# Performance work log

Measured on AMD Instinct MI355X. Metric: run time of the kernel, lower is better.

The kernel has to match this reference:

```python
import jax, jax.numpy as jnp
import numpy as np

N = 100000   # nodes
E = 1600000  # edges (avg degree 16)
IN_DIM = 5
HID = 128
OUT_DIM = 1


def gcn_conv(x, src, dst, W, b, n):
    """PyG GCNConv: out = D^{-1/2}(A+I)D^{-1/2} (x @ W) + b, self-loops added."""
    h = x @ W  # [N, F_out]
    # degree including self-loop (edge weight 1 each)
    deg = jax.ops.segment_sum(jnp.ones(src.shape[0], h.dtype), dst, num_segments=n) + 1.0
    dinv = jax.lax.rsqrt(deg)  # deg >= 1 always (self-loop)
    coef = dinv[src] * dinv[dst]  # [E]
    agg = jax.ops.segment_sum(h[src] * coef[:, None], dst, num_segments=n)
    agg = agg + h * (dinv * dinv)[:, None]  # self-loop contribution
    return agg + b


def setup_inputs() -> dict:
    key = jax.random.key(0)
    k = jax.random.split(key, 6)
    x = jax.random.normal(k[0], (N, IN_DIM), jnp.float32)
    edge_index = jax.random.randint(k[1], (2, E), 0, N)
    W1 = jax.random.normal(k[2], (IN_DIM, HID), jnp.float32) / np.float32(np.sqrt(IN_DIM))
    b1 = jnp.zeros((HID,), jnp.float32)
    W2 = jax.random.normal(k[3], (HID, OUT_DIM), jnp.float32) / np.float32(np.sqrt(HID))
    b2 = jnp.zeros((OUT_DIM,), jnp.float32)
    return {"x": x, "edge_index": edge_index, "W1": W1, "b1": b1, "W2": W2, "b2": b2}


def reference(x, edge_index, W1, b1, W2, b2):
    src, dst = edge_index[0], edge_index[1]
    h = gcn_conv(x, src, dst, W1, b1, N)
    h = jax.nn.relu(h)
    out = gcn_conv(h, src, dst, W2, b2, N)
    return out
```

## Files before the change

### kernel.cpp

```cpp
#include <hip/hip_runtime.h>
#include <hip/hip_fp16.h>

#define Nn 100000
#define Ee 1600000
#define HID 128
#define IN_DIM 5

#define SH 8
#define BSZ 256
#define NB 391
#define BCAP 4608

#define PCHUNK 4000
#define PBLK (Ee / PCHUNK)

typedef float f32x4 __attribute__((ext_vector_type(4)));
union F2H { float f; __half2 h; };

__global__ void zero_kernel(int* __restrict__ bcnt) {
    if (threadIdx.x < NB) bcnt[threadIdx.x] = 0;
}

__global__ __launch_bounds__(512) void partition_kernel(const int* __restrict__ src,
                                                        const int* __restrict__ dst,
                                                        unsigned int* __restrict__ recs,
                                                        int* __restrict__ bcnt) {
    __shared__ unsigned int stage[PCHUNK];
    __shared__ int hist[NB + 1];
    __shared__ int cur[NB];
    __shared__ int gbase[NB];
    int e0 = blockIdx.x * PCHUNK;
    for (int i = threadIdx.x; i <= NB; i += 512) hist[i] = 0;
    __syncthreads();
    for (int e = e0 + threadIdx.x; e < e0 + PCHUNK; e += 512)
        atomicAdd(&hist[(dst[e] >> SH) + 1], 1);
    __syncthreads();
    if (threadIdx.x == 0)
        for (int b = 1; b <= NB; ++b) hist[b] += hist[b - 1];
    __syncthreads();
    if (threadIdx.x < NB) {
        int c0 = hist[threadIdx.x], c1 = hist[threadIdx.x + 1];
        cur[threadIdx.x] = c0;
        gbase[threadIdx.x] = atomicAdd(&bcnt[threadIdx.x], c1 - c0);
    }
    __syncthreads();
    for (int e = e0 + threadIdx.x; e < e0 + PCHUNK; e += 512) {
        int d = dst[e], s = src[e];
        int b = d >> SH;
        int slot = atomicAdd(&cur[b], 1);
        stage[slot] = ((unsigned int)(d & (BSZ - 1)) << 17) | (unsigned int)s;
    }
    __syncthreads();
    int wave = threadIdx.x >> 6, lane = threadIdx.x & 63;
    for (int b = wave; b < NB; b += 8) {
        int c0 = hist[b], len = hist[b + 1] - c0;
        unsigned int* o = recs + (size_t)b * BCAP + gbase[b];
        for (int i = lane; i < len; i += 64) o[i] = stage[c0 + i];
    }
}

__global__ __launch_bounds__(BSZ) void sortk_kernel(const unsigned int* __restrict__ recs,
                                                    const int* __restrict__ bcnt,
                                                    const float* __restrict__ x,
                                                    int* __restrict__ degc,
                                                    unsigned int* __restrict__ nodeoff,
                                                    unsigned int* __restrict__ ssrc,
                                                    float* __restrict__ dinv,
                                                    f32x4* __restrict__ xd16) {
    __shared__ int cnt[BSZ];
    __shared__ int cur[BSZ];
    __shared__ int wsum[BSZ / 64];
    int b = blockIdx.x, tid = threadIdx.x;
    int n = bcnt[b];
    cnt[tid] = 0;
    __syncthreads();
    const unsigned int* R = recs + (size_t)b * BCAP;
    for (int i = tid; i < n; i += BSZ)
        atomicAdd(&cnt[R[i] >> 17], 1);
    __syncthreads();
    int v = cnt[tid];
    int lane = tid & 63, wid = tid >> 6;
    int sc = v;
    #pragma unroll
    for (int ofs = 1; ofs < 64; ofs <<= 1) {
        int t = __shfl_up(sc, ofs, 64);
        if (lane >= ofs) sc += t;
    }
    if (lane == 63) wsum[wid] = sc;
    __syncthreads();
    int wpre = 0;
    #pragma unroll
    for (int w = 0; w < BSZ / 64; ++w)
        if (w < wid) wpre += wsum[w];
    int excl = wpre + sc - v;
    cur[tid] = excl;
    int g = (b << SH) + tid;
    if (g < Nn) {
        degc[g] = v;
        nodeoff[g] = (unsigned int)(b * BCAP + excl);
        float di = rsqrtf((float)v + 1.0f);
        dinv[g] = di;
        f32x4 o;
        o.x = x[g * IN_DIM + 0] * di;
        o.y = x[g * IN_DIM + 1] * di;
        o.z = x[g * IN_DIM + 2] * di;
        F2H u;
        u.h = __floats2half2_rn(x[g * IN_DIM + 3] * di, x[g * IN_DIM + 4] * di);
        o.w = u.f;
        xd16[g] = o;
    }
    __syncthreads();
    unsigned int* O = ssrc + (size_t)b * BCAP;
    for (int i = tid; i < n; i += BSZ) {
        unsigned int r = R[i];
        int pos = atomicAdd(&cur[r >> 17], 1);
        O[pos] = r & 0x1FFFFu;
    }
}

__global__ __launch_bounds__(256) void gcn1_kernel(const unsigned int* __restrict__ ssrc,
                                                   const unsigned int* __restrict__ nodeoff,
                                                   const int* __restrict__ degc,
                                                   const f32x4* __restrict__ xd16,
                                                   const float* __restrict__ dinv,
                                                   const float* __restrict__ W1,
                                                   const float* __restrict__ b1,
                                                   const float* __restrict__ W2,
                                                   float* __restrict__ h2d) {
    __shared__ float w1s[IN_DIM * HID];
    __shared__ float w2s[HID], b1s[HID];
    int tid = threadIdx.x;
    for (int j = tid; j < IN_DIM * HID; j += 256) w1s[j] = W1[j];
    if (tid < HID) { w2s[tid] = W2[tid]; b1s[tid] = b1[tid]; }
    __syncthreads();
    int nd = blockIdx.x * 256 + tid;
    if (nd >= Nn) return;
    unsigned int off = nodeoff[nd];
    int len = degc[nd];
    float a0 = 0.f, a1 = 0.f, a2 = 0.f, a3 = 0.f, a4 = 0.f;
    int i = 0;
    for (; i + 4 <= len; i += 4) {
        unsigned int s0 = ssrc[off + i], s1 = ssrc[off + i + 1];
        unsigned int s2 = ssrc[off + i + 2], s3 = ssrc[off + i + 3];
        f32x4 v0 = xd16[s0], v1 = xd16[s1], v2 = xd16[s2], v3 = xd16[s3];
        F2H u0, u1, u2, u3;
        u0.f = v0.w; u1.f = v1.w; u2.f = v2.w; u3.f = v3.w;
        float2 e0 = __half22float2(u0.h), e1 = __half22float2(u1.h);
        float2 e2 = __half22float2(u2.h), e3 = __half22float2(u3.h);
        a0 += (v0.x + v1.x) + (v2.x + v3.x);
        a1 += (v0.y + v1.y) + (v2.y + v3.y);
        a2 += (v0.z + v1.z) + (v2.z + v3.z);
        a3 += (e0.x + e1.x) + (e2.x + e3.x);
        a4 += (e0.y + e1.y) + (e2.y + e3.y);
    }
    for (; i < len; ++i) {
        unsigned int s = ssrc[off + i];
        f32x4 v = xd16[s];
        F2H u; u.f = v.w; float2 e = __half22float2(u.h);
        a0 += v.x; a1 += v.y; a2 += v.z; a3 += e.x; a4 += e.y;
    }
    float di = dinv[nd];
    f32x4 sv = xd16[nd];
    F2H su; su.f = sv.w; float2 se = __half22float2(su.h);
    a0 = (a0 + sv.x) * di;
    a1 = (a1 + sv.y) * di;
    a2 = (a2 + sv.z) * di;
    a3 = (a3 + se.x) * di;
    a4 = (a4 + se.y) * di;
    float accp = 0.f;
    #pragma unroll
    for (int f = 0; f < HID; ++f) {
        float v = b1s[f] + a0 * w1s[f] + a1 * w1s[HID + f] + a2 * w1s[2 * HID + f]
                + a3 * w1s[3 * HID + f] + a4 * w1s[4 * HID + f];
        accp += fmaxf(v, 0.f) * w2s[f];
    }
    h2d[nd] = accp * di;
}

__global__ __launch_bounds__(256) void gcn2_kernel(const unsigned int* __restrict__ ssrc,
                                                   const unsigned int* __restrict__ nodeoff,
                                                   const int* __restrict__ degc,
                                                   const float* __restrict__ h2d,
                                                   const float* __restrict__ dinv,
                                                   const float* __restrict__ b2,
                                                   float* __restrict__ out) {
    int nd = blockIdx.x * 256 + threadIdx.x;
    if (nd >= Nn) return;
    unsigned int off = nodeoff[nd];
    int len = degc[nd];
    float s = 0.f;
    int i = 0;
    for (; i + 8 <= len; i += 8) {
        float t0 = h2d[ssrc[off + i]],     t1 = h2d[ssrc[off + i + 1]];
        float t2 = h2d[ssrc[off + i + 2]], t3 = h2d[ssrc[off + i + 3]];
        float t4 = h2d[ssrc[off + i + 4]], t5 = h2d[ssrc[off + i + 5]];
        float t6 = h2d[ssrc[off + i + 6]], t7 = h2d[ssrc[off + i + 7]];
        s += ((t0 + t1) + (t2 + t3)) + ((t4 + t5) + (t6 + t7));
    }
    for (; i < len; ++i) s += h2d[ssrc[off + i]];
    out[nd] = (s + h2d[nd]) * dinv[nd] + b2[0];
}

extern "C" void kernel_launch(void* const* d_in, const int* in_sizes, int n_in,
                              void* d_out, int out_size, void* d_ws, size_t ws_size,
                              hipStream_t stream) {
    const float* x  = (const float*)d_in[0];
    const int*   ei = (const int*)d_in[1];
    const float* W1 = (const float*)d_in[2];
    const float* b1 = (const float*)d_in[3];
    const float* W2 = (const float*)d_in[4];
    const float* b2 = (const float*)d_in[5];
    const int* src = ei;
    const int* dst = ei + Ee;
    float* out = (float*)d_out;

    float* dinv = (float*)d_ws;
    f32x4* xd16 = (f32x4*)(dinv + Nn);
    float* h2d  = (float*)(xd16 + Nn);
    int* degc   = (int*)(h2d + Nn);
    unsigned int* nodeoff = (unsigned int*)(degc + Nn);
    unsigned int* recs = nodeoff + Nn;
    unsigned int* ssrc = recs + (size_t)NB * BCAP;
    int* bcnt = (int*)(ssrc + (size_t)NB * BCAP);

    zero_kernel<<<1, 512, 0, stream>>>(bcnt);
    partition_kernel<<<PBLK, 512, 0, stream>>>(src, dst, recs, bcnt);
    sortk_kernel<<<NB, BSZ, 0, stream>>>(recs, bcnt, x, degc, nodeoff, ssrc, dinv, xd16);
    gcn1_kernel<<<(Nn + 255) / 256, 256, 0, stream>>>(ssrc, nodeoff, degc, xd16, dinv,
                                                      W1, b1, W2, h2d);
    gcn2_kernel<<<(Nn + 255) / 256, 256, 0, stream>>>(ssrc, nodeoff, degc, h2d, dinv, b2, out);
}
```

Measured before the change: 81.87 us.

## Restructure edge partition: register-cached edges, parallel scan, flat coalesced scatter

The partition kernel now loads each edge's src/dst once into registers (up to 7 per thread) instead of reading dst twice from global memory. The serial single-thread prefix sum over 391 buckets becomes a wave-shuffle scan. The per-wave bucket copy-out becomes a flat loop over staged records, using an extra shared bucket-id array. Chunk size changes to 3125 with 512 blocks for better occupancy and more blocks in flight, at the cost of more global atomics on bucket counters.

Result: faster. 70.21 us (-14.2%).

```diff
diff --git a/kernel.cpp b/kernel.cpp
--- a/kernel.cpp
+++ b/kernel.cpp
@@ -11,8 +11,9 @@
 #define NB 391
 #define BCAP 4608
 
-#define PCHUNK 4000
-#define PBLK (Ee / PCHUNK)
+#define PCHUNK 3125
+#define PBLK 512
+#define MAXK 7
 
 typedef float f32x4 __attribute__((ext_vector_type(4)));
 union F2H { float f; __half2 h; };
@@ -26,36 +27,63 @@
                                                         unsigned int* __restrict__ recs,
                                                         int* __restrict__ bcnt) {
     __shared__ unsigned int stage[PCHUNK];
+    __shared__ unsigned short bstage[PCHUNK];
     __shared__ int hist[NB + 1];
+    __shared__ int histS[NB + 1];
     __shared__ int cur[NB];
     __shared__ int gbase[NB];
+    __shared__ int wsum[8];
+    int tid = threadIdx.x;
     int e0 = blockIdx.x * PCHUNK;
-    for (int i = threadIdx.x; i <= NB; i += 512) hist[i] = 0;
-    __syncthreads();
-    for (int e = e0 + threadIdx.x; e < e0 + PCHUNK; e += 512)
-        atomicAdd(&hist[(dst[e] >> SH) + 1], 1);
-    __syncthreads();
-    if (threadIdx.x == 0)
-        for (int b = 1; b <= NB; ++b) hist[b] += hist[b - 1];
-    __syncthreads();
-    if (threadIdx.x < NB) {
-        int c0 = hist[threadIdx.x], c1 = hist[threadIdx.x + 1];
-        cur[threadIdx.x] = c0;
-        gbase[threadIdx.x] = atomicAdd(&bcnt[threadIdx.x], c1 - c0);
-    }
-    __syncthreads();
-    for (int e = e0 + threadIdx.x; e < e0 + PCHUNK; e += 512) {
-        int d = dst[e], s = src[e];
-        int b = d >> SH;
-        int slot = atomicAdd(&cur[b], 1);
-        stage[slot] = ((unsigned int)(d & (BSZ - 1)) << 17) | (unsigned int)s;
-    }
-    __syncthreads();
-    int wave = threadIdx.x >> 6, lane = threadIdx.x & 63;
-    for (int b = wave; b < NB; b += 8) {
-        int c0 = hist[b], len = hist[b + 1] - c0;
-        unsigned int* o = recs + (size_t)b * BCAP + gbase[b];
-        for (int i = lane; i < len; i += 64) o[i] = stage[c0 + i];
+    for (int i = tid; i <= NB; i += 512) hist[i] = 0;
+    __syncthreads();
+    int rb[MAXK];
+    unsigned int rv[MAXK];
+    #pragma unroll
+    for (int k = 0; k < MAXK; ++k) {
+        int idx = tid + k * 512;
+        rb[k] = -1;
+        if (idx < PCHUNK) {
+            int e = e0 + idx;
+            int d = dst[e], s = src[e];
+            rb[k] = d >> SH;
+            rv[k] = ((unsigned int)(d & (BSZ - 1)) << 17) | (unsigned int)s;
+            atomicAdd(&hist[rb[k]], 1);
+        }
+    }
+    __syncthreads();
+    int v = (tid < NB) ? hist[tid] : 0;
+    int lane = tid & 63, wid = tid >> 6;
+    int sc = v;
+    #pragma unroll
+    for (int ofs = 1; ofs < 64; ofs <<= 1) {
+        int t = __shfl_up(sc, ofs, 64);
+        if (lane >= ofs) sc += t;
+    }
+    if (lane == 63) wsum[wid] = sc;
+    __syncthreads();
+    int wpre = 0;
+    #pragma unroll
+    for (int w = 0; w < 8; ++w)
+        if (w < wid) wpre += wsum[w];
+    int excl = wpre + sc - v;
+    if (tid < NB) {
+        histS[tid] = excl;
+        cur[tid] = excl;
+        gbase[tid] = atomicAdd(&bcnt[tid], v);
+    }
+    __syncthreads();
+    #pragma unroll
+    for (int k = 0; k < MAXK; ++k)
+        if (rb[k] >= 0) {
+            int slot = atomicAdd(&cur[rb[k]], 1);
+            stage[slot] = rv[k];
+            bstage[slot] = (unsigned short)rb[k];
+        }
+    __syncthreads();
+    for (int i = tid; i < PCHUNK; i += 512) {
+        int b = bstage[i];
+        recs[(size_t)b * BCAP + gbase[b] + (i - histS[b])] = stage[i];
     }
 }
 
```

## Replace two-pass bucket partition sort with global atomic counting-sort CSR build

Applied to the files above, without the earlier changes.

Replaces the shared-memory bucketed partition plus per-bucket local sort with a classic global counting sort. Degrees come from global atomics on dst, block-level scans take their bases from a global atomic allocator, and a fill pass scatters src into slots via per-node atomic cursors. This removes the intermediate record buffer and one full pass over the edges. In exchange it uses 1.6M contended global atomics twice, and the scattered writes lose the locality of the bucketed approach. Node segments are now allocated in non-deterministic block order, and edge order within a node is non-deterministic.

Result: slower. 196.3 us (+139.8%).

```diff
diff --git a/kernel.cpp b/kernel.cpp
--- a/kernel.cpp
+++ b/kernel.cpp
@@ -6,79 +6,41 @@
 #define HID 128
 #define IN_DIM 5
 
-#define SH 8
-#define BSZ 256
-#define NB 391
-#define BCAP 4608
-
-#define PCHUNK 4000
-#define PBLK (Ee / PCHUNK)
+#define GBLK 800
+#define GTHR 512
+#define GSTR (GBLK * GTHR)
 
 typedef float f32x4 __attribute__((ext_vector_type(4)));
 union F2H { float f; __half2 h; };
 
-__global__ void zero_kernel(int* __restrict__ bcnt) {
-    if (threadIdx.x < NB) bcnt[threadIdx.x] = 0;
-}
-
-__global__ __launch_bounds__(512) void partition_kernel(const int* __restrict__ src,
-                                                        const int* __restrict__ dst,
-                                                        unsigned int* __restrict__ recs,
-                                                        int* __restrict__ bcnt) {
-    __shared__ unsigned int stage[PCHUNK];
-    __shared__ int hist[NB + 1];
-    __shared__ int cur[NB];
-    __shared__ int gbase[NB];
-    int e0 = blockIdx.x * PCHUNK;
-    for (int i = threadIdx.x; i <= NB; i += 512) hist[i] = 0;
-    __syncthreads();
-    for (int e = e0 + threadIdx.x; e < e0 + PCHUNK; e += 512)
-        atomicAdd(&hist[(dst[e] >> SH) + 1], 1);
-    __syncthreads();
-    if (threadIdx.x == 0)
-        for (int b = 1; b <= NB; ++b) hist[b] += hist[b - 1];
-    __syncthreads();
-    if (threadIdx.x < NB) {
-        int c0 = hist[threadIdx.x], c1 = hist[threadIdx.x + 1];
-        cur[threadIdx.x] = c0;
-        gbase[threadIdx.x] = atomicAdd(&bcnt[threadIdx.x], c1 - c0);
-    }
-    __syncthreads();
-    for (int e = e0 + threadIdx.x; e < e0 + PCHUNK; e += 512) {
-        int d = dst[e], s = src[e];
-        int b = d >> SH;
-        int slot = atomicAdd(&cur[b], 1);
-        stage[slot] = ((unsigned int)(d & (BSZ - 1)) << 17) | (unsigned int)s;
-    }
-    __syncthreads();
-    int wave = threadIdx.x >> 6, lane = threadIdx.x & 63;
-    for (int b = wave; b < NB; b += 8) {
-        int c0 = hist[b], len = hist[b + 1] - c0;
-        unsigned int* o = recs + (size_t)b * BCAP + gbase[b];
-        for (int i = lane; i < len; i += 64) o[i] = stage[c0 + i];
-    }
-}
-
-__global__ __launch_bounds__(BSZ) void sortk_kernel(const unsigned int* __restrict__ recs,
-                                                    const int* __restrict__ bcnt,
-                                                    const float* __restrict__ x,
-                                                    int* __restrict__ degc,
-                                                    unsigned int* __restrict__ nodeoff,
-                                                    unsigned int* __restrict__ ssrc,
-                                                    float* __restrict__ dinv,
-                                                    f32x4* __restrict__ xd16) {
-    __shared__ int cnt[BSZ];
-    __shared__ int cur[BSZ];
-    __shared__ int wsum[BSZ / 64];
-    int b = blockIdx.x, tid = threadIdx.x;
-    int n = bcnt[b];
-    cnt[tid] = 0;
-    __syncthreads();
-    const unsigned int* R = recs + (size_t)b * BCAP;
-    for (int i = tid; i < n; i += BSZ)
-        atomicAdd(&cnt[R[i] >> 17], 1);
-    __syncthreads();
-    int v = cnt[tid];
+__global__ __launch_bounds__(256) void zero_kernel(int* __restrict__ degc,
+                                                   unsigned int* __restrict__ galloc) {
+    int i = blockIdx.x * 256 + threadIdx.x;
+    if (i < Nn) degc[i] = 0;
+    if (i == 0) *galloc = 0u;
+}
+
+__global__ __launch_bounds__(GTHR) void count_kernel(const int* __restrict__ dst,
+                                                     int* __restrict__ degc) {
+    int t = blockIdx.x * GTHR + threadIdx.x;
+    #pragma unroll
+    for (int k = 0; k < 4; ++k) {
+        int e = t + k * GSTR;
+        if (e < Ee) atomicAdd(&degc[dst[e]], 1);
+    }
+}
+
+__global__ __launch_bounds__(256) void scan_prep_kernel(const int* __restrict__ degc,
+                                                        const float* __restrict__ x,
+                                                        unsigned int* __restrict__ cursor,
+                                                        float* __restrict__ dinv,
+                                                        f32x4* __restrict__ xd16,
+                                                        unsigned int* __restrict__ galloc) {
+    __shared__ int wsum[4];
+    __shared__ unsigned int bbase;
+    int tid = threadIdx.x;
+    int nd = blockIdx.x * 256 + tid;
+    int v = (nd < Nn) ? degc[nd] : 0;
     int lane = tid & 63, wid = tid >> 6;
     int sc = v;
     #pragma unroll
@@ -88,38 +50,54 @@
     }
     if (lane == 63) wsum[wid] = sc;
     __syncthreads();
+    if (tid == 0) {
+        int bt = wsum[0] + wsum[1] + wsum[2] + wsum[3];
+        bbase = atomicAdd(galloc, (unsigned int)bt);
+    }
+    __syncthreads();
     int wpre = 0;
     #pragma unroll
-    for (int w = 0; w < BSZ / 64; ++w)
+    for (int w = 0; w < 4; ++w)
         if (w < wid) wpre += wsum[w];
-    int excl = wpre + sc - v;
-    cur[tid] = excl;
-    int g = (b << SH) + tid;
-    if (g < Nn) {
-        degc[g] = v;
-        nodeoff[g] = (unsigned int)(b * BCAP + excl);
+    if (nd < Nn) {
+        cursor[nd] = bbase + (unsigned int)(wpre + sc - v);
         float di = rsqrtf((float)v + 1.0f);
-        dinv[g] = di;
+        dinv[nd] = di;
         f32x4 o;
-        o.x = x[g * IN_DIM + 0] * di;
-        o.y = x[g * IN_DIM + 1] * di;
-        o.z = x[g * IN_DIM + 2] * di;
+        o.x = x[nd * IN_DIM + 0] * di;
+        o.y = x[nd * IN_DIM + 1] * di;
+        o.z = x[nd * IN_DIM + 2] * di;
         F2H u;
-        u.h = __floats2half2_rn(x[g * IN_DIM + 3] * di, x[g * IN_DIM + 4] * di);
+        u.h = __floats2half2_rn(x[nd * IN_DIM + 3] * di, x[nd * IN_DIM + 4] * di);
         o.w = u.f;
-        xd16[g] = o;
-    }
-    __syncthreads();
-    unsigned int* O = ssrc + (size_t)b * BCAP;
-    for (int i = tid; i < n; i += BSZ) {
-        unsigned int r = R[i];
-        int pos = atomicAdd(&cur[r >> 17], 1);
-        O[pos] = r & 0x1FFFFu;
-    }
+        xd16[nd] = o;
+    }
+}
+
+__global__ __launch_bounds__(GTHR) void fill_kernel(const int* __restrict__ src,
+                                                    const int* __restrict__ dst,
+                                                    unsigned int* __restrict__ cursor,
+                                                    unsigned int* __restrict__ ssrc) {
+    int t = blockIdx.x * GTHR + threadIdx.x;
+    int d[4], s[4];
+    bool ok[4];
+    #pragma unroll
+    for (int k = 0; k < 4; ++k) {
+        int e = t + k * GSTR;
+        ok[k] = (e < Ee);
+        if (ok[k]) { d[k] = dst[e]; s[k] = src[e]; }
+    }
+    unsigned int slot[4];
+    #pragma unroll
+    for (int k = 0; k < 4; ++k)
+        if (ok[k]) slot[k] = atomicAdd(&cursor[d[k]], 1u);
+    #pragma unroll
+    for (int k = 0; k < 4; ++k)
+        if (ok[k]) ssrc[slot[k]] = (unsigned int)s[k];
 }
 
 __global__ __launch_bounds__(256) void gcn1_kernel(const unsigned int* __restrict__ ssrc,
-                                                   const unsigned int* __restrict__ nodeoff,
+                                                   const unsigned int* __restrict__ cursor,
                                                    const int* __restrict__ degc,
                                                    const f32x4* __restrict__ xd16,
                                                    const float* __restrict__ dinv,
@@ -135,8 +113,8 @@
     __syncthreads();
     int nd = blockIdx.x * 256 + tid;
     if (nd >= Nn) return;
-    unsigned int off = nodeoff[nd];
     int len = degc[nd];
+    unsigned int off = cursor[nd] - (unsigned int)len;
     float a0 = 0.f, a1 = 0.f, a2 = 0.f, a3 = 0.f, a4 = 0.f;
     int i = 0;
     for (; i + 4 <= len; i += 4) {
@@ -178,7 +156,7 @@
 }
 
 __global__ __launch_bounds__(256) void gcn2_kernel(const unsigned int* __restrict__ ssrc,
-                                                   const unsigned int* __restrict__ nodeoff,
+                                                   const unsigned int* __restrict__ cursor,
                                                    const int* __restrict__ degc,
                                                    const float* __restrict__ h2d,
                                                    const float* __restrict__ dinv,
@@ -186,8 +164,8 @@
                                                    float* __restrict__ out) {
     int nd = blockIdx.x * 256 + threadIdx.x;
     if (nd >= Nn) return;
-    unsigned int off = nodeoff[nd];
     int len = degc[nd];
+    unsigned int off = cursor[nd] - (unsigned int)len;
     float s = 0.f;
     int i = 0;
     for (; i + 8 <= len; i += 8) {
@@ -218,15 +196,15 @@
     f32x4* xd16 = (f32x4*)(dinv + Nn);
     float* h2d  = (float*)(xd16 + Nn);
     int* degc   = (int*)(h2d + Nn);
-    unsigned int* nodeoff = (unsigned int*)(degc + Nn);
-    unsigned int* recs = nodeoff + Nn;
-    unsigned int* ssrc = recs + (size_t)NB * BCAP;
-    int* bcnt = (int*)(ssrc + (size_t)NB * BCAP);
-
-    zero_kernel<<<1, 512, 0, stream>>>(bcnt);
-    partition_kernel<<<PBLK, 512, 0, stream>>>(src, dst, recs, bcnt);
-    sortk_kernel<<<NB, BSZ, 0, stream>>>(recs, bcnt, x, degc, nodeoff, ssrc, dinv, xd16);
-    gcn1_kernel<<<(Nn + 255) / 256, 256, 0, stream>>>(ssrc, nodeoff, degc, xd16, dinv,
+    unsigned int* cursor = (unsigned int*)(degc + Nn);
+    unsigned int* ssrc = cursor + Nn;
+    unsigned int* galloc = ssrc + Ee;
+
+    zero_kernel<<<(Nn + 255) / 256, 256, 0, stream>>>(degc, galloc);
+    count_kernel<<<GBLK, GTHR, 0, stream>>>(dst, degc);
+    scan_prep_kernel<<<(Nn + 255) / 256, 256, 0, stream>>>(degc, x, cursor, dinv, xd16, galloc);
+    fill_kernel<<<GBLK, GTHR, 0, stream>>>(src, dst, cursor, ssrc);
+    gcn1_kernel<<<(Nn + 255) / 256, 256, 0, stream>>>(ssrc, cursor, degc, xd16, dinv,
                                                       W1, b1, W2, h2d);
-    gcn2_kernel<<<(Nn + 255) / 256, 256, 0, stream>>>(ssrc, nodeoff, degc, h2d, dinv, b2, out);
-}
+    gcn2_kernel<<<(Nn + 255) / 256, 256, 0, stream>>>(ssrc, cursor, degc, h2d, dinv, b2, out);
+}
```
